# Kernel optimization log

Measured on AMD Instinct MI355X. Metric: run time of the kernel, lower is better.

## Reference

```python
import jax, jax.numpy as jnp
import numpy as np

N = 50000   # nodes
E = 800000  # edges (avg degree 16)
D = 64      # in_feat
OUT = 64    # out_feat


def _layernorm(x, gamma, beta, eps=1e-5):
    m = jnp.mean(x, axis=-1, keepdims=True)
    v = jnp.mean((x - m) ** 2, axis=-1, keepdims=True)  # biased var, as torch LayerNorm
    return (x - m) * jax.lax.rsqrt(v + eps) * gamma + beta


def setup_inputs() -> dict:
    key = jax.random.key(0)
    ks = jax.random.split(key, 6)
    s1 = 1.0 / np.sqrt(D)
    s2 = 1.0 / np.sqrt(2 * D)
    return {
        "x": jax.random.normal(ks[0], (N, D), dtype=jnp.float32),
        "edge_index": jax.random.randint(ks[1], (2, E), 0, N, dtype=jnp.int64),
        "W1a": jax.random.normal(ks[2], (D, D), dtype=jnp.float32) * s1,
        "W1b": jax.random.normal(ks[3], (D, D), dtype=jnp.float32) * s1,
        "gamma1": jnp.ones((D,), jnp.float32),
        "beta1": jnp.zeros((D,), jnp.float32),
        "w": jnp.ones((D,), jnp.float32),
        "gamma2": jnp.ones((D,), jnp.float32),
        "beta2": jnp.zeros((D,), jnp.float32),
        "W2a": jax.random.normal(ks[4], (D, 2 * D), dtype=jnp.float32) * s2,
        "W2b": jax.random.normal(ks[5], (OUT, D), dtype=jnp.float32) * s1,
    }


def reference(x, edge_index, W1a, W1b, gamma1, beta1, w, gamma2, beta2, W2a, W2b):
    row, col = edge_index[0], edge_index[1]
    n = x.shape[0]
    # gather -> MLP1 (two bias-free linears with ReLU)
    msg = x[row]                                        # [E, D]
    msg = jax.nn.relu(msg @ W1a.T) @ W1b.T              # [E, D]
    # scatter_mean over destination nodes
    s = jax.ops.segment_sum(msg, col, num_segments=n)   # [N, D]
    cnt = jax.ops.segment_sum(jnp.ones((col.shape[0],), x.dtype), col, num_segments=n)
    agg = s / jnp.maximum(cnt, 1.0)[:, None]
    agg = _layernorm(agg, gamma1, beta1)
    # repulsion + residual + LayerNorm
    fx = _layernorm(x + (x - agg) * w, gamma2, beta2)
    # concat -> MLP2
    h = jnp.concatenate([fx, agg], axis=1)              # [N, 2D]
    return jax.nn.relu(h @ W2a.T) @ W2b.T               # [N, OUT]
```

## Files before the change

### kernel.cpp

```cpp
#include <hip/hip_runtime.h>
#include <hip/hip_bf16.h>

#define NN 50000
#define NE 800000
#define CAP 48
#define BINS 196
#define P1B 98
#define CHUNK 8164
#define MLPB 768
#define SUPT 782

typedef short v8s __attribute__((ext_vector_type(8)));
typedef float v4f __attribute__((ext_vector_type(4)));
#define MFMA16(a, b, c) __builtin_amdgcn_mfma_f32_16x16x32_bf16(a, b, c, 0, 0, 0)

__device__ __forceinline__ float bfu2f(unsigned short u) {
    union { unsigned int i; float f; } v; v.i = ((unsigned int)u) << 16; return v.f;
}
__device__ __forceinline__ unsigned short f2bf_rne(float f) {
    union { float f; unsigned int i; } v; v.f = f;
    unsigned int x = v.i;
    unsigned int r = x + 0x7fffu + ((x >> 16) & 1u);
    return (unsigned short)(r >> 16);
}
__device__ __forceinline__ v8s fragf32(const float* p) {
    float4 u = ((const float4*)p)[0];
    float4 v = ((const float4*)p)[1];
    v8s r;
    r[0] = (short)f2bf_rne(u.x); r[1] = (short)f2bf_rne(u.y);
    r[2] = (short)f2bf_rne(u.z); r[3] = (short)f2bf_rne(u.w);
    r[4] = (short)f2bf_rne(v.x); r[5] = (short)f2bf_rne(v.y);
    r[6] = (short)f2bf_rne(v.z); r[7] = (short)f2bf_rne(v.w);
    return r;
}
__device__ __forceinline__ v8s fragbf(const unsigned short* p) {
    union { uint4 u; v8s s; } t; t.u = *((const uint4*)p); return t.s;
}
__device__ __forceinline__ v4f vzero() { v4f z; z[0]=0.f; z[1]=0.f; z[2]=0.f; z[3]=0.f; return z; }

__global__ __launch_bounds__(256) void p1fat_k(const int* __restrict__ ei,
                                               const float* __restrict__ x,
                                               const float* __restrict__ W1a,
                                               const float* __restrict__ W1b,
                                               unsigned int* __restrict__ chunkbuf,
                                               unsigned short* __restrict__ histT,
                                               unsigned short* __restrict__ y) {
    __shared__ unsigned int smem[8616];
    int t = threadIdx.x;
    if (blockIdx.x < P1B) {
        unsigned int* hcnt = smem;
        unsigned int* scan = smem + BINS;
        unsigned int* data = smem + BINS + 256;
        int p = blockIdx.x;
        int e0 = p * CHUNK;
        int e1 = e0 + CHUNK; if (e1 > NE) e1 = NE;
        int ne = e1 - e0;
        bool i64 = ((ei[1] | ei[3] | ei[5] | ei[7]) == 0);
        for (int i = t; i < BINS; i += 256) hcnt[i] = 0;
        __syncthreads();
        unsigned int packed[32];
#pragma unroll
        for (int i = 0; i < 32; ++i) {
            int e = e0 + t + 256 * i;
            unsigned int pk = 0xFFFFFFFFu;
            if (e < e1) {
                int col = i64 ? ei[2 * (NE + e)] : ei[NE + e];
                int row = i64 ? ei[2 * e]        : ei[e];
                pk = ((unsigned int)col << 16) | (unsigned int)row;
                atomicAdd(&hcnt[col >> 8], 1u);
            }
            packed[i] = pk;
        }
        __syncthreads();
        scan[t] = (t < BINS) ? hcnt[t] : 0;
        __syncthreads();
        for (int off = 1; off < 256; off <<= 1) {
            unsigned int a = (t >= off) ? scan[t - off] : 0;
            __syncthreads();
            scan[t] += a;
            __syncthreads();
        }
        if (t < BINS) {
            unsigned int st = scan[t] - hcnt[t];
            scan[t] = st;
            hcnt[t] = st;
        }
        __syncthreads();
#pragma unroll
        for (int i = 0; i < 32; ++i) {
            unsigned int pk = packed[i];
            if (pk != 0xFFFFFFFFu) {
                unsigned int pos = atomicAdd(&hcnt[pk >> 24], 1u);
                data[pos] = pk;
            }
        }
        __syncthreads();
        unsigned int* cb = chunkbuf + (size_t)p * CHUNK;
        for (int i = t; i < ne; i += 256) cb[i] = data[i];
        for (int i = t; i < BINS; i += 256)
            histT[i * P1B + p] = (unsigned short)scan[i];
        return;
    }
    unsigned short* wa  = (unsigned short*)smem;
    unsigned short* wb  = wa + 64 * 72;
    unsigned short* h1s = wb + 64 * 72;
    for (int i = t; i < 64 * 64; i += 256) {
        int r = i >> 6, c = i & 63;
        wa[r * 72 + c] = f2bf_rne(W1a[i]);
        wb[r * 72 + c] = f2bf_rne(W1b[i]);
    }
    __syncthreads();
    int w = t >> 6, l = t & 63;
    int lm = l & 15, lq = l >> 4;
    for (int st = blockIdx.x - P1B; st < SUPT; st += MLPB) {
        int nb = st * 64;
        int arow = nb + w * 16 + lm;
        int arc = arow < NN ? arow : NN - 1;
        const float* xr = x + (size_t)arc * 64;
        v8s a0 = fragf32(xr + lq * 8);
        v8s a1 = fragf32(xr + 32 + lq * 8);
        v4f acc[4];
#pragma unroll
        for (int jt = 0; jt < 4; ++jt) acc[jt] = vzero();
#pragma unroll
        for (int jt = 0; jt < 4; ++jt) {
            const unsigned short* wr = &wa[(jt * 16 + lm) * 72];
            acc[jt] = MFMA16(a0, fragbf(wr + lq * 8), acc[jt]);
            acc[jt] = MFMA16(a1, fragbf(wr + 32 + lq * 8), acc[jt]);
        }
#pragma unroll
        for (int jt = 0; jt < 4; ++jt)
#pragma unroll
            for (int r = 0; r < 4; ++r)
                h1s[(w * 16 + lq * 4 + r) * 72 + jt * 16 + lm] = f2bf_rne(fmaxf(acc[jt][r], 0.0f));
        __syncthreads();
        v8s c0 = fragbf(&h1s[(w * 16 + lm) * 72 + lq * 8]);
        v8s c1 = fragbf(&h1s[(w * 16 + lm) * 72 + 32 + lq * 8]);
        v4f acc2[4];
#pragma unroll
        for (int jt = 0; jt < 4; ++jt) acc2[jt] = vzero();
#pragma unroll
        for (int jt = 0; jt < 4; ++jt) {
            const unsigned short* wr = &wb[(jt * 16 + lm) * 72];
            acc2[jt] = MFMA16(c0, fragbf(wr + lq * 8), acc2[jt]);
            acc2[jt] = MFMA16(c1, fragbf(wr + 32 + lq * 8), acc2[jt]);
        }
#pragma unroll
        for (int jt = 0; jt < 4; ++jt)
#pragma unroll
            for (int r = 0; r < 4; ++r) {
                int n = nb + w * 16 + lq * 4 + r;
                if (n < NN) y[(size_t)n * 64 + jt * 16 + lm] = f2bf_rne(acc2[jt][r]);
            }
        __syncthreads();
    }
}

__global__ __launch_bounds__(256) void p2_k(const unsigned int* __restrict__ chunkbuf,
                                            const unsigned short* __restrict__ histT,
                                            unsigned short* __restrict__ bucket1,
                                            int* __restrict__ cnt) {
    __shared__ unsigned int cl[256];
    __shared__ unsigned short dl[256 * CAP];
    __shared__ unsigned int scan[128];
    __shared__ unsigned short sstart[P1B];
    __shared__ unsigned short base[P1B];
    int t = threadIdx.x;
    int b = blockIdx.x;
    int c0 = b << 8;
    for (int i = t; i < 256; i += 256) cl[i] = 0;
    for (int i = t; i < 256 * CAP / 2; i += 256) ((unsigned int*)dl)[i] = 0;
    unsigned int len = 0;
    if (t < P1B) {
        unsigned int st = histT[b * P1B + t];
        int ne = NE - t * CHUNK; if (ne > CHUNK) ne = CHUNK;
        unsigned int en = (b == BINS - 1) ? (unsigned int)ne : histT[(b + 1) * P1B + t];
        len = en - st;
        sstart[t] = (unsigned short)st;
    }
    if (t < 128) scan[t] = (t < P1B) ? len : 0;
    __syncthreads();
    for (int off = 1; off < 128; off <<= 1) {
        unsigned int a = (t < 128 && t >= off) ? scan[t - off] : 0;
        __syncthreads();
        if (t < 128) scan[t] += a;
        __syncthreads();
    }
    if (t < P1B) base[t] = (unsigned short)(scan[t] - len);
    __syncthreads();
    int tot = (int)scan[P1B - 1];
    for (int k = t; k < tot; k += 256) {
        int lo = 0, hi = P1B - 1;
#pragma unroll
        for (int it = 0; it < 7; ++it) {
            int mid = (lo + hi + 1) >> 1;
            if ((int)base[mid] <= k) lo = mid; else hi = mid - 1;
        }
        int idx = (int)sstart[lo] + (k - (int)base[lo]);
        unsigned int d = chunkbuf[(size_t)lo * CHUNK + idx];
        int c = (int)(d >> 16) - c0;
        unsigned int slot = atomicAdd(&cl[c], 1u);
        if (slot < CAP) dl[c * CAP + slot] = (unsigned short)(d & 0xffffu);
    }
    __syncthreads();
    for (int i = t; i < 256; i += 256)
        if (c0 + i < NN) cnt[c0 + i] = (int)cl[i];
    uint4* dst = (uint4*)(bucket1 + (size_t)c0 * CAP);
    const uint4* src = (const uint4*)dl;
    for (int i = t; i < 256 * CAP / 8; i += 256) dst[i] = src[i];
}

__device__ __forceinline__ float wsum64(float v) {
#pragma unroll
    for (int o = 32; o > 0; o >>= 1) v += __shfl_xor(v, o, 64);
    return v;
}
__device__ __forceinline__ void ln_store(float s0, float s1, int tdeg, int n, int p, int j, int f0,
                                         const float* __restrict__ x,
                                         const float* __restrict__ g1, const float* __restrict__ b1,
                                         const float* __restrict__ wrep,
                                         const float* __restrict__ g2, const float* __restrict__ b2,
                                         unsigned short* __restrict__ h) {
    float inv = 1.0f / (float)(tdeg > 1 ? tdeg : 1);
    float a0 = s0 * inv, a1 = s1 * inv;
    float m = wsum64(a0 + a1) * (1.0f / 128.0f);
    float d0 = a0 - m, d1 = a1 - m;
    float var = wsum64(d0 * d0 + d1 * d1) * (1.0f / 128.0f);
    float r = rsqrtf(var + 1e-5f);
    float2 g1v = *(const float2*)(g1 + f0);
    float2 b1v = *(const float2*)(b1 + f0);
    a0 = d0 * r * g1v.x + b1v.x;
    a1 = d1 * r * g1v.y + b1v.y;
    float2 xv = *(const float2*)(x + (size_t)n * 64 + f0);
    float2 wv = *(const float2*)(wrep + f0);
    float t0 = xv.x + (xv.x - a0) * wv.x;
    float t1 = xv.y + (xv.y - a1) * wv.y;
    float m2 = wsum64(t0 + t1) * (1.0f / 128.0f);
    float e0 = t0 - m2, e1 = t1 - m2;
    float var2 = wsum64(e0 * e0 + e1 * e1) * (1.0f / 128.0f);
    float r2 = rsqrtf(var2 + 1e-5f);
    float2 g2v = *(const float2*)(g2 + f0);
    float2 b2v = *(const float2*)(b2 + f0);
    float fx0 = e0 * r2 * g2v.x + b2v.x;
    float fx1 = e1 * r2 * g2v.y + b2v.y;
    unsigned* hw = (unsigned*)(h + (size_t)n * 128);
    if (p == 0) hw[j]      = (unsigned)f2bf_rne(fx0) | ((unsigned)f2bf_rne(fx1) << 16);
    else        hw[32 + j] = (unsigned)f2bf_rne(a0)  | ((unsigned)f2bf_rne(a1)  << 16);
}
__global__ __launch_bounds__(256) void gathernorm_k(const int* __restrict__ cnt,
                                                    const unsigned short* __restrict__ bucket1,
                                                    const unsigned short* __restrict__ y,
                                                    const float* __restrict__ x,
                                                    const float* __restrict__ g1, const float* __restrict__ b1,
                                                    const float* __restrict__ wrep,
                                                    const float* __restrict__ g2, const float* __restrict__ b2,
                                                    unsigned short* __restrict__ h) {
    int n0 = blockIdx.x * 8 + (threadIdx.x >> 6) * 2;
    if (n0 >= NN) return;
    int n1 = n0 + 1;
    int n1c = n1 < NN ? n1 : n0;
    int l = threadIdx.x & 63;
    int p = l >> 5;
    int j = l & 31;
    int f0 = 2 * j;
    int dA = cnt[n0], dB = cnt[n1c];
    int eA = dA < CAP ? dA : CAP;
    int eB = dB < CAP ? dB : CAP;
    const uint4* bpA = (const uint4*)(bucket1 + (size_t)n0 * CAP);
    const uint4* bpB = (const uint4*)(bucket1 + (size_t)n1c * CAP);
    uint4 qA[6], qB[6];
#pragma unroll
    for (int i = 0; i < 6; ++i) { qA[i] = bpA[i]; qB[i] = bpB[i]; }
    float sA0 = 0.f, sA1 = 0.f, sB0 = 0.f, sB1 = 0.f;
#pragma unroll
    for (int c = 0; c < 6; ++c) {
        bool cA = c * 8 < eA, cB = c * 8 < eB;
        if (cA | cB) {
            unsigned wA[4] = { qA[c].x, qA[c].y, qA[c].z, qA[c].w };
            unsigned wB[4] = { qB[c].x, qB[c].y, qB[c].z, qB[c].w };
#pragma unroll
            for (int i = 0; i < 4; ++i) {
                int e = c * 8 + 2 * i + p;
                int idA = (int)((wA[i] >> (p * 16)) & 0xffffu);
                int idB = (int)((wB[i] >> (p * 16)) & 0xffffu);
                unsigned uA = *(const unsigned*)(y + (size_t)idA * 64 + f0);
                unsigned uB = *(const unsigned*)(y + (size_t)idB * 64 + f0);
                bool okA = cA && e < eA, okB = cB && e < eB;
                sA0 += okA ? bfu2f((unsigned short)(uA & 0xffffu)) : 0.0f;
                sA1 += okA ? bfu2f((unsigned short)(uA >> 16)) : 0.0f;
                sB0 += okB ? bfu2f((unsigned short)(uB & 0xffffu)) : 0.0f;
                sB1 += okB ? bfu2f((unsigned short)(uB >> 16)) : 0.0f;
            }
        }
    }
    sA0 += __shfl_xor(sA0, 32, 64);
    sA1 += __shfl_xor(sA1, 32, 64);
    sB0 += __shfl_xor(sB0, 32, 64);
    sB1 += __shfl_xor(sB1, 32, 64);
    ln_store(sA0, sA1, dA, n0, p, j, f0, x, g1, b1, wrep, g2, b2, h);
    if (n1 < NN)
        ln_store(sB0, sB1, dB, n1, p, j, f0, x, g1, b1, wrep, g2, b2, h);
}

__global__ __launch_bounds__(256) void mlp2_k(const unsigned short* hin,
                                              const float* __restrict__ W2a,
                                              const float* __restrict__ W2b,
                                              float* out) {
    __shared__ unsigned short sm2[64 * 136 + 64 * 72 + 64 * 72];
    unsigned short* wa2 = sm2;
    unsigned short* wb2 = wa2 + 64 * 136;
    unsigned short* t2s = wb2 + 64 * 72;
    int t = threadIdx.x;
    for (int i = t; i < 64 * 128; i += 256) {
        int r = i >> 7, c = i & 127;
        wa2[r * 136 + c] = f2bf_rne(W2a[i]);
    }
    for (int i = t; i < 64 * 64; i += 256) {
        int r = i >> 6, c = i & 63;
        wb2[r * 72 + c] = f2bf_rne(W2b[i]);
    }
    __syncthreads();
    int w = t >> 6, l = t & 63;
    int lm = l & 15, lq = l >> 4;
    for (int st = blockIdx.x; st < SUPT; st += MLPB) {
        int nb = st * 64;
        int arow = nb + w * 16 + lm;
        int arc = arow < NN ? arow : NN - 1;
        const unsigned short* fr = hin + (size_t)arc * 128;
        v8s a0 = fragbf(fr + lq * 8);
        v8s a1 = fragbf(fr + 32 + lq * 8);
        v8s a2 = fragbf(fr + 64 + lq * 8);
        v8s a3 = fragbf(fr + 96 + lq * 8);
        v4f acc[4];
#pragma unroll
        for (int jt = 0; jt < 4; ++jt) acc[jt] = vzero();
#pragma unroll
        for (int jt = 0; jt < 4; ++jt) {
            const unsigned short* wr = &wa2[(jt * 16 + lm) * 136];
            acc[jt] = MFMA16(a0, fragbf(wr + lq * 8), acc[jt]);
            acc[jt] = MFMA16(a1, fragbf(wr + 32 + lq * 8), acc[jt]);
            acc[jt] = MFMA16(a2, fragbf(wr + 64 + lq * 8), acc[jt]);
            acc[jt] = MFMA16(a3, fragbf(wr + 96 + lq * 8), acc[jt]);
        }
#pragma unroll
        for (int jt = 0; jt < 4; ++jt)
#pragma unroll
            for (int r = 0; r < 4; ++r)
                t2s[(w * 16 + lq * 4 + r) * 72 + jt * 16 + lm] = f2bf_rne(fmaxf(acc[jt][r], 0.0f));
        __syncthreads();
        v8s c0 = fragbf(&t2s[(w * 16 + lm) * 72 + lq * 8]);
        v8s c1 = fragbf(&t2s[(w * 16 + lm) * 72 + 32 + lq * 8]);
        v4f acc2[4];
#pragma unroll
        for (int jt = 0; jt < 4; ++jt) acc2[jt] = vzero();
#pragma unroll
        for (int jt = 0; jt < 4; ++jt) {
            const unsigned short* wr = &wb2[(jt * 16 + lm) * 72];
            acc2[jt] = MFMA16(c0, fragbf(wr + lq * 8), acc2[jt]);
            acc2[jt] = MFMA16(c1, fragbf(wr + 32 + lq * 8), acc2[jt]);
        }
#pragma unroll
        for (int jt = 0; jt < 4; ++jt)
#pragma unroll
            for (int r = 0; r < 4; ++r) {
                int n = nb + w * 16 + lq * 4 + r;
                if (n < NN) out[(size_t)n * 64 + jt * 16 + lm] = acc2[jt][r];
            }
        __syncthreads();
    }
}

extern "C" void kernel_launch(void* const* d_in, const int* in_sizes, int n_in,
                              void* d_out, int out_size, void* d_ws, size_t ws_size,
                              hipStream_t stream) {
    const float* x   = (const float*)d_in[0];
    const int*   ei  = (const int*)d_in[1];
    const float* W1a = (const float*)d_in[2];
    const float* W1b = (const float*)d_in[3];
    const float* g1  = (const float*)d_in[4];
    const float* b1  = (const float*)d_in[5];
    const float* w   = (const float*)d_in[6];
    const float* g2  = (const float*)d_in[7];
    const float* b2  = (const float*)d_in[8];
    const float* W2a = (const float*)d_in[9];
    const float* W2b = (const float*)d_in[10];

    char* ws = (char*)d_ws;
    unsigned short* y        = (unsigned short*)(ws + 0);
    unsigned int*   chunkbuf = (unsigned int*)(ws + 6400000);
    unsigned short* histT    = (unsigned short*)(ws + 9600288);
    unsigned short* bucket1  = (unsigned short*)(ws + 9638720);
    int*            cnt      = (int*)(ws + 14455616);

    p1fat_k<<<P1B + MLPB, 256, 0, stream>>>(ei, x, W1a, W1b, chunkbuf, histT, y);
    p2_k<<<BINS, 256, 0, stream>>>(chunkbuf, histT, bucket1, cnt);
    gathernorm_k<<<(NN + 7) / 8, 256, 0, stream>>>(cnt, bucket1, y, x,
                                                   g1, b1, w, g2, b2, (unsigned short*)d_out);
    mlp2_k<<<MLPB, 256, 0, stream>>>((const unsigned short*)d_out, W2a, W2b, (float*)d_out);
    (void)in_sizes; (void)n_in; (void)out_size; (void)ws_size;
}
```

Baseline: 152.3 us.

## Fuse gather-normalize with MLP2, keeping concatenated features in LDS

Merges the gather/LayerNorm kernel and the MLP2 kernel into one kernel. Each block handles 64 nodes, writes the bf16 [fx, agg] rows into shared memory, then runs the MFMA MLP directly on them. This removes one launch and the global round trip of the intermediate h buffer. W2a/W2b are now read as fp32 from global per fragment rather than staged as bf16 in LDS, which adds redundant weight loads and conversions per block, and each wave now walks 16 nodes serially, which lowers parallelism in the gather phase.

```diff
diff --git a/kernel.cpp b/kernel.cpp
--- a/kernel.cpp
+++ b/kernel.cpp
@@ -215,12 +215,13 @@
     for (int o = 32; o > 0; o >>= 1) v += __shfl_xor(v, o, 64);
     return v;
 }
-__device__ __forceinline__ void ln_store(float s0, float s1, int tdeg, int n, int p, int j, int f0,
-                                         const float* __restrict__ x,
-                                         const float* __restrict__ g1, const float* __restrict__ b1,
-                                         const float* __restrict__ wrep,
-                                         const float* __restrict__ g2, const float* __restrict__ b2,
-                                         unsigned short* __restrict__ h) {
+__device__ __forceinline__ void ln_store_lds(float s0, float s1, int tdeg, int nc, int ln,
+                                             int p, int j, int f0,
+                                             const float* __restrict__ x,
+                                             const float* __restrict__ g1, const float* __restrict__ b1,
+                                             const float* __restrict__ wrep,
+                                             const float* __restrict__ g2, const float* __restrict__ b2,
+                                             unsigned short* __restrict__ hs) {
     float inv = 1.0f / (float)(tdeg > 1 ? tdeg : 1);
     float a0 = s0 * inv, a1 = s1 * inv;
     float m = wsum64(a0 + a1) * (1.0f / 128.0f);
@@ -231,7 +232,7 @@
     float2 b1v = *(const float2*)(b1 + f0);
     a0 = d0 * r * g1v.x + b1v.x;
     a1 = d1 * r * g1v.y + b1v.y;
-    float2 xv = *(const float2*)(x + (size_t)n * 64 + f0);
+    float2 xv = *(const float2*)(x + (size_t)nc * 64 + f0);
     float2 wv = *(const float2*)(wrep + f0);
     float t0 = xv.x + (xv.x - a0) * wv.x;
     float t1 = xv.y + (xv.y - a1) * wv.y;
@@ -243,131 +244,113 @@
     float2 b2v = *(const float2*)(b2 + f0);
     float fx0 = e0 * r2 * g2v.x + b2v.x;
     float fx1 = e1 * r2 * g2v.y + b2v.y;
-    unsigned* hw = (unsigned*)(h + (size_t)n * 128);
+    unsigned* hw = (unsigned*)(hs + ln * 136);
     if (p == 0) hw[j]      = (unsigned)f2bf_rne(fx0) | ((unsigned)f2bf_rne(fx1) << 16);
     else        hw[32 + j] = (unsigned)f2bf_rne(a0)  | ((unsigned)f2bf_rne(a1)  << 16);
 }
-__global__ __launch_bounds__(256) void gathernorm_k(const int* __restrict__ cnt,
-                                                    const unsigned short* __restrict__ bucket1,
-                                                    const unsigned short* __restrict__ y,
-                                                    const float* __restrict__ x,
-                                                    const float* __restrict__ g1, const float* __restrict__ b1,
-                                                    const float* __restrict__ wrep,
-                                                    const float* __restrict__ g2, const float* __restrict__ b2,
-                                                    unsigned short* __restrict__ h) {
-    int n0 = blockIdx.x * 8 + (threadIdx.x >> 6) * 2;
-    if (n0 >= NN) return;
-    int n1 = n0 + 1;
-    int n1c = n1 < NN ? n1 : n0;
-    int l = threadIdx.x & 63;
+__global__ __launch_bounds__(256) void gml_k(const int* __restrict__ cnt,
+                                             const unsigned short* __restrict__ bucket1,
+                                             const unsigned short* __restrict__ y,
+                                             const float* __restrict__ x,
+                                             const float* __restrict__ g1, const float* __restrict__ b1,
+                                             const float* __restrict__ wrep,
+                                             const float* __restrict__ g2, const float* __restrict__ b2,
+                                             const float* __restrict__ W2a,
+                                             const float* __restrict__ W2b,
+                                             float* __restrict__ out) {
+    __shared__ unsigned short hs[64 * 136];
+    __shared__ unsigned short t2s[64 * 72];
+    int nb = blockIdx.x * 64;
+    int t = threadIdx.x;
+    int w = t >> 6, l = t & 63;
     int p = l >> 5;
     int j = l & 31;
     int f0 = 2 * j;
-    int dA = cnt[n0], dB = cnt[n1c];
-    int eA = dA < CAP ? dA : CAP;
-    int eB = dB < CAP ? dB : CAP;
-    const uint4* bpA = (const uint4*)(bucket1 + (size_t)n0 * CAP);
-    const uint4* bpB = (const uint4*)(bucket1 + (size_t)n1c * CAP);
-    uint4 qA[6], qB[6];
-#pragma unroll
-    for (int i = 0; i < 6; ++i) { qA[i] = bpA[i]; qB[i] = bpB[i]; }
-    float sA0 = 0.f, sA1 = 0.f, sB0 = 0.f, sB1 = 0.f;
-#pragma unroll
-    for (int c = 0; c < 6; ++c) {
-        bool cA = c * 8 < eA, cB = c * 8 < eB;
-        if (cA | cB) {
-            unsigned wA[4] = { qA[c].x, qA[c].y, qA[c].z, qA[c].w };
-            unsigned wB[4] = { qB[c].x, qB[c].y, qB[c].z, qB[c].w };
-#pragma unroll
-            for (int i = 0; i < 4; ++i) {
-                int e = c * 8 + 2 * i + p;
-                int idA = (int)((wA[i] >> (p * 16)) & 0xffffu);
-                int idB = (int)((wB[i] >> (p * 16)) & 0xffffu);
-                unsigned uA = *(const unsigned*)(y + (size_t)idA * 64 + f0);
-                unsigned uB = *(const unsigned*)(y + (size_t)idB * 64 + f0);
-                bool okA = cA && e < eA, okB = cB && e < eB;
-                sA0 += okA ? bfu2f((unsigned short)(uA & 0xffffu)) : 0.0f;
-                sA1 += okA ? bfu2f((unsigned short)(uA >> 16)) : 0.0f;
-                sB0 += okB ? bfu2f((unsigned short)(uB & 0xffffu)) : 0.0f;
-                sB1 += okB ? bfu2f((unsigned short)(uB >> 16)) : 0.0f;
+#pragma unroll 1
+    for (int pr = 0; pr < 8; ++pr) {
+        int n0 = nb + w * 16 + pr * 2;
+        int n1 = n0 + 1;
+        int n0c = n0 < NN ? n0 : NN - 1;
+        int n1c = n1 < NN ? n1 : NN - 1;
+        int dA = cnt[n0c], dB = cnt[n1c];
+        int eA = dA < CAP ? dA : CAP;
+        int eB = dB < CAP ? dB : CAP;
+        const uint4* bpA = (const uint4*)(bucket1 + (size_t)n0c * CAP);
+        const uint4* bpB = (const uint4*)(bucket1 + (size_t)n1c * CAP);
+        uint4 qA[6], qB[6];
+#pragma unroll
+        for (int i = 0; i < 6; ++i) { qA[i] = bpA[i]; qB[i] = bpB[i]; }
+        float sA0 = 0.f, sA1 = 0.f, sB0 = 0.f, sB1 = 0.f;
+#pragma unroll
+        for (int c = 0; c < 6; ++c) {
+            bool cA = c * 8 < eA, cB = c * 8 < eB;
+            if (cA | cB) {
+                unsigned wA[4] = { qA[c].x, qA[c].y, qA[c].z, qA[c].w };
+                unsigned wB[4] = { qB[c].x, qB[c].y, qB[c].z, qB[c].w };
+#pragma unroll
+                for (int i = 0; i < 4; ++i) {
+                    int e = c * 8 + 2 * i + p;
+                    int idA = (int)((wA[i] >> (p * 16)) & 0xffffu);
+                    int idB = (int)((wB[i] >> (p * 16)) & 0xffffu);
+                    unsigned uA = *(const unsigned*)(y + (size_t)idA * 64 + f0);
+                    unsigned uB = *(const unsigned*)(y + (size_t)idB * 64 + f0);
+                    bool okA = cA && e < eA, okB = cB && e < eB;
+                    sA0 += okA ? bfu2f((unsigned short)(uA & 0xffffu)) : 0.0f;
+                    sA1 += okA ? bfu2f((unsigned short)(uA >> 16)) : 0.0f;
+                    sB0 += okB ? bfu2f((unsigned short)(uB & 0xffffu)) : 0.0f;
+                    sB1 += okB ? bfu2f((unsigned short)(uB >> 16)) : 0.0f;
+                }
             }
         }
-    }
-    sA0 += __shfl_xor(sA0, 32, 64);
-    sA1 += __shfl_xor(sA1, 32, 64);
-    sB0 += __shfl_xor(sB0, 32, 64);
-    sB1 += __shfl_xor(sB1, 32, 64);
-    ln_store(sA0, sA1, dA, n0, p, j, f0, x, g1, b1, wrep, g2, b2, h);
-    if (n1 < NN)
-        ln_store(sB0, sB1, dB, n1, p, j, f0, x, g1, b1, wrep, g2, b2, h);
-}
-
-__global__ __launch_bounds__(256) void mlp2_k(const unsigned short* hin,
-                                              const float* __restrict__ W2a,
-                                              const float* __restrict__ W2b,
-                                              float* out) {
-    __shared__ unsigned short sm2[64 * 136 + 64 * 72 + 64 * 72];
-    unsigned short* wa2 = sm2;
-    unsigned short* wb2 = wa2 + 64 * 136;
-    unsigned short* t2s = wb2 + 64 * 72;
-    int t = threadIdx.x;
-    for (int i = t; i < 64 * 128; i += 256) {
-        int r = i >> 7, c = i & 127;
-        wa2[r * 136 + c] = f2bf_rne(W2a[i]);
-    }
-    for (int i = t; i < 64 * 64; i += 256) {
-        int r = i >> 6, c = i & 63;
-        wb2[r * 72 + c] = f2bf_rne(W2b[i]);
-    }
-    __syncthreads();
-    int w = t >> 6, l = t & 63;
+        sA0 += __shfl_xor(sA0, 32, 64);
+        sA1 += __shfl_xor(sA1, 32, 64);
+        sB0 += __shfl_xor(sB0, 32, 64);
+        sB1 += __shfl_xor(sB1, 32, 64);
+        ln_store_lds(sA0, sA1, dA, n0c, n0 - nb, p, j, f0, x, g1, b1, wrep, g2, b2, hs);
+        ln_store_lds(sB0, sB1, dB, n1c, n1 - nb, p, j, f0, x, g1, b1, wrep, g2, b2, hs);
+    }
+    __syncthreads();
     int lm = l & 15, lq = l >> 4;
-    for (int st = blockIdx.x; st < SUPT; st += MLPB) {
-        int nb = st * 64;
-        int arow = nb + w * 16 + lm;
-        int arc = arow < NN ? arow : NN - 1;
-        const unsigned short* fr = hin + (size_t)arc * 128;
-        v8s a0 = fragbf(fr + lq * 8);
-        v8s a1 = fragbf(fr + 32 + lq * 8);
-        v8s a2 = fragbf(fr + 64 + lq * 8);
-        v8s a3 = fragbf(fr + 96 + lq * 8);
-        v4f acc[4];
-#pragma unroll
-        for (int jt = 0; jt < 4; ++jt) acc[jt] = vzero();
-#pragma unroll
-        for (int jt = 0; jt < 4; ++jt) {
-            const unsigned short* wr = &wa2[(jt * 16 + lm) * 136];
-            acc[jt] = MFMA16(a0, fragbf(wr + lq * 8), acc[jt]);
-            acc[jt] = MFMA16(a1, fragbf(wr + 32 + lq * 8), acc[jt]);
-            acc[jt] = MFMA16(a2, fragbf(wr + 64 + lq * 8), acc[jt]);
-            acc[jt] = MFMA16(a3, fragbf(wr + 96 + lq * 8), acc[jt]);
-        }
-#pragma unroll
-        for (int jt = 0; jt < 4; ++jt)
-#pragma unroll
-            for (int r = 0; r < 4; ++r)
-                t2s[(w * 16 + lq * 4 + r) * 72 + jt * 16 + lm] = f2bf_rne(fmaxf(acc[jt][r], 0.0f));
-        __syncthreads();
-        v8s c0 = fragbf(&t2s[(w * 16 + lm) * 72 + lq * 8]);
-        v8s c1 = fragbf(&t2s[(w * 16 + lm) * 72 + 32 + lq * 8]);
-        v4f acc2[4];
-#pragma unroll
-        for (int jt = 0; jt < 4; ++jt) acc2[jt] = vzero();
-#pragma unroll
-        for (int jt = 0; jt < 4; ++jt) {
-            const unsigned short* wr = &wb2[(jt * 16 + lm) * 72];
-            acc2[jt] = MFMA16(c0, fragbf(wr + lq * 8), acc2[jt]);
-            acc2[jt] = MFMA16(c1, fragbf(wr + 32 + lq * 8), acc2[jt]);
-        }
-#pragma unroll
-        for (int jt = 0; jt < 4; ++jt)
-#pragma unroll
-            for (int r = 0; r < 4; ++r) {
-                int n = nb + w * 16 + lq * 4 + r;
-                if (n < NN) out[(size_t)n * 64 + jt * 16 + lm] = acc2[jt][r];
-            }
-        __syncthreads();
-    }
+    const unsigned short* fr = &hs[(w * 16 + lm) * 136];
+    v8s a0 = fragbf(fr + lq * 8);
+    v8s a1 = fragbf(fr + 32 + lq * 8);
+    v8s a2 = fragbf(fr + 64 + lq * 8);
+    v8s a3 = fragbf(fr + 96 + lq * 8);
+    v4f acc[4];
+#pragma unroll
+    for (int jt = 0; jt < 4; ++jt) acc[jt] = vzero();
+#pragma unroll
+    for (int jt = 0; jt < 4; ++jt) {
+        const float* wr = W2a + (size_t)(jt * 16 + lm) * 128;
+        acc[jt] = MFMA16(a0, fragf32(wr + lq * 8), acc[jt]);
+        acc[jt] = MFMA16(a1, fragf32(wr + 32 + lq * 8), acc[jt]);
+        acc[jt] = MFMA16(a2, fragf32(wr + 64 + lq * 8), acc[jt]);
+        acc[jt] = MFMA16(a3, fragf32(wr + 96 + lq * 8), acc[jt]);
+    }
+#pragma unroll
+    for (int jt = 0; jt < 4; ++jt)
+#pragma unroll
+        for (int r = 0; r < 4; ++r)
+            t2s[(w * 16 + lq * 4 + r) * 72 + jt * 16 + lm] = f2bf_rne(fmaxf(acc[jt][r], 0.0f));
+    __syncthreads();
+    v8s c0 = fragbf(&t2s[(w * 16 + lm) * 72 + lq * 8]);
+    v8s c1 = fragbf(&t2s[(w * 16 + lm) * 72 + 32 + lq * 8]);
+    v4f acc2[4];
+#pragma unroll
+    for (int jt = 0; jt < 4; ++jt) acc2[jt] = vzero();
+#pragma unroll
+    for (int jt = 0; jt < 4; ++jt) {
+        const float* wr = W2b + (size_t)(jt * 16 + lm) * 64;
+        acc2[jt] = MFMA16(c0, fragf32(wr + lq * 8), acc2[jt]);
+        acc2[jt] = MFMA16(c1, fragf32(wr + 32 + lq * 8), acc2[jt]);
+    }
+#pragma unroll
+    for (int jt = 0; jt < 4; ++jt)
+#pragma unroll
+        for (int r = 0; r < 4; ++r) {
+            int n = nb + w * 16 + lq * 4 + r;
+            if (n < NN) out[(size_t)n * 64 + jt * 16 + lm] = acc2[jt][r];
+        }
 }
 
 extern "C" void kernel_launch(void* const* d_in, const int* in_sizes, int n_in,
@@ -394,8 +377,7 @@
 
     p1fat_k<<<P1B + MLPB, 256, 0, stream>>>(ei, x, W1a, W1b, chunkbuf, histT, y);
     p2_k<<<BINS, 256, 0, stream>>>(chunkbuf, histT, bucket1, cnt);
-    gathernorm_k<<<(NN + 7) / 8, 256, 0, stream>>>(cnt, bucket1, y, x,
-                                                   g1, b1, w, g2, b2, (unsigned short*)d_out);
-    mlp2_k<<<MLPB, 256, 0, stream>>>((const unsigned short*)d_out, W2a, W2b, (float*)d_out);
+    gml_k<<<SUPT, 256, 0, stream>>>(cnt, bucket1, y, x, g1, b1, w, g2, b2,
+                                    W2a, W2b, (float*)d_out);
     (void)in_sizes; (void)n_in; (void)out_size; (void)ws_size;
 }
```

Measured after the change: 204.6 us. 34.3% more time.
